# Kernel tuning notes

Hardware: AMD Instinct MI355X
Metric: run time of the kernel (lower is better)

The kernel has to match this reference:

```python
import jax, jax.numpy as jnp
import numpy as np

D_OUT = 512          # full_tensor_dims[0]
VIEW_DIMS = (512, 512, 512)
RANK = 32
BATCH = 4096


def _xavier(key, shape):
    # xavier-style init: scale by sqrt(2 / (fan_in + fan_out)) over first/last dims
    fan_in, fan_out = shape[0] * shape[1], shape[2]
    scale = jnp.sqrt(2.0 / (fan_in + fan_out)).astype(jnp.float32)
    return jax.random.normal(key, shape, dtype=jnp.float32) * scale


def setup_inputs() -> dict:
    key = jax.random.key(0)
    ks = jax.random.split(key, 8)
    X0 = jax.random.normal(ks[0], (VIEW_DIMS[0], BATCH), dtype=jnp.float32)
    X1 = jax.random.normal(ks[1], (VIEW_DIMS[1], BATCH), dtype=jnp.float32)
    X2 = jax.random.normal(ks[2], (VIEW_DIMS[2], BATCH), dtype=jnp.float32)
    # TT cores: rank chain [1, 32, 32, 32, 1]
    core0 = _xavier(ks[3], (1, D_OUT, RANK))            # [1, d_out, r1]
    core1 = _xavier(ks[4], (RANK, VIEW_DIMS[0], RANK))  # [r1, d1, r2]
    core2 = _xavier(ks[5], (RANK, VIEW_DIMS[1], RANK))  # [r2, d2, r3]
    core3 = _xavier(ks[6], (RANK, VIEW_DIMS[2], 1))     # [r3, d3, 1]
    return {"X0": X0, "X1": X1, "X2": X2,
            "core0": core0, "core1": core1, "core2": core2, "core3": core3}


def reference(X0, X1, X2, core0, core1, core2, core3):
    # Batched equivalent of the per-sample Python loop in TensorTrain.forward.
    # For each view j: M_j[n] = mode_dot(core_{j+1}^T_{0,2,1}, X_j[:, n], mode=2)
    #   == einsum('adb,dn->nab'), shape [B, r_{j+1}, r_{j+2}]
    Xs = (X0, X1, X2)
    chain_cores = (core1, core2, core3)
    Ms = [jnp.einsum('adb,dn->nab', c, x) for c, x in zip(chain_cores, Xs)]
    # Chain of per-sample matmuls: z = M_0 @ M_1 @ M_2 -> [B, r1, 1]
    acc = Ms[0]
    for M in Ms[1:]:
        acc = jnp.einsum('nab,nbc->nac', acc, M)
    # Z[:, n] = mode_dot(core0, z[:, 0], mode=2)[0, :]
    Z = jnp.einsum('oda,na->dn', core0, acc[:, :, 0])  # [d_out, B]
    return Z


if __name__ == '__main__':
    out = reference(**setup_inputs())
    print(out.shape)
```

## Files before the change

### kernel.cpp

```cpp
#include <hip/hip_runtime.h>

#define D 512
#define B 4096
#define R 32
#define AB 1024

typedef unsigned short ushort_t;
typedef __attribute__((ext_vector_type(8))) short bf16x8;
typedef __attribute__((ext_vector_type(4))) float f32x4;

__device__ __forceinline__ ushort_t f2bf(float f) {
  uint32_t u = __builtin_bit_cast(uint32_t, f);
  u = (u + 0x7FFFu + ((u >> 16) & 1u)) >> 16;
  return (ushort_t)u;
}
__device__ __forceinline__ float bf2f(ushort_t h) {
  uint32_t u = ((uint32_t)h) << 16;
  return __builtin_bit_cast(float, u);
}
__device__ __forceinline__ void gload_lds16(const void* g, void* lds) {
  __builtin_amdgcn_global_load_lds(
      (const __attribute__((address_space(1))) unsigned int*)g,
      (__attribute__((address_space(3))) unsigned int*)lds, 16, 0, 0);
}

__global__ __launch_bounds__(256) void prep(
    const float* __restrict__ X0, const float* __restrict__ X1,
    const float* __restrict__ X2, const float* __restrict__ c1,
    const float* __restrict__ c2, const float* __restrict__ c3,
    ushort_t* __restrict__ Xt, ushort_t* __restrict__ Apack,
    ushort_t* __restrict__ Apack3)
{
  __shared__ __align__(16) char smem[33280];
  const int bid = blockIdx.x, tid = threadIdx.x;

  if (bid < 1536) {
    float (*T)[65] = (float(*)[65])smem;
    const int v = bid / 512, tile = bid % 512;
    const float* __restrict__ X = (v == 0) ? X0 : ((v == 1) ? X1 : X2);
    ushort_t* __restrict__ O = Xt + (size_t)v * B * D;
    const int n0 = (tile & 63) * 64, d0 = (tile >> 6) * 64;
#pragma unroll
    for (int i = 0; i < 16; ++i) {
      int e = i * 256 + tid;
      T[e >> 6][e & 63] = X[(size_t)(d0 + (e >> 6)) * B + n0 + (e & 63)];
    }
    __syncthreads();
#pragma unroll
    for (int i = 0; i < 2; ++i) {
      int ch = i * 256 + tid;
      int nr = ch >> 3, dc = (ch & 7) * 8;
      ushort_t w[8];
#pragma unroll
      for (int q = 0; q < 8; ++q) w[q] = f2bf(T[dc + q][nr]);
      *(bf16x8*)&O[(size_t)(n0 + nr) * D + d0 + dc] = *(bf16x8*)w;
    }
  } else if (bid < 1600) {
    ushort_t (*T)[D + 8] = (ushort_t(*)[D + 8])smem;
    const int ja = bid - 1536, j = ja >> 5, a = ja & 31;
    const float* __restrict__ c = j ? c2 : c1;
#pragma unroll
    for (int i = 0; i < 64; ++i) {
      int e = i * 256 + tid;
      T[e & 31][e >> 5] = f2bf(c[(size_t)a * (D * R) + e]);
    }
    __syncthreads();
#pragma unroll
    for (int i = 0; i < 8; ++i) {
      int ch = i * 256 + tid;
      int b = ch >> 6, off = (ch & 63) * 8;
      ushort_t w[8];
#pragma unroll
      for (int q = 0; q < 8; ++q) w[q] = T[b][off + q];
      *(bf16x8*)&Apack[((size_t)j * AB + a * 32 + b) * D + off] = *(bf16x8*)w;
    }
  } else {
    const int r0 = (bid - 1600) * 16;
#pragma unroll
    for (int i = 0; i < 4; ++i) {
      int ch = i * 256 + tid;
      int rr = r0 + (ch >> 6), off = (ch & 63) * 8;
      ushort_t w[8];
      if (rr < R) {
#pragma unroll
        for (int q = 0; q < 8; ++q) w[q] = f2bf(c3[(size_t)rr * D + off + q]);
      } else {
#pragma unroll
        for (int q = 0; q < 8; ++q) w[q] = 0;
      }
      *(bf16x8*)&Apack3[(size_t)rr * D + off] = *(bf16x8*)w;
    }
  }
}

__global__ __launch_bounds__(256) void gemm_mfma(
    const ushort_t* __restrict__ Apack, const ushort_t* __restrict__ Apack3,
    const ushort_t* __restrict__ Xt, ushort_t* __restrict__ Mt,
    ushort_t* __restrict__ Mt2)
{
  __shared__ __align__(16) ushort_t smem[17408];
  ushort_t* As0 = smem;
  ushort_t* As1 = smem + 4096;
  ushort_t* Bs0 = smem + 8192;
  ushort_t* Bs1 = smem + 12288;

  const int bid = blockIdx.x;
  int j, rb, nb, ldc;
  const ushort_t *Ag, *Bg;
  ushort_t* C;
  if (bid < 512) {
    j = bid >> 8; int w = bid & 255; rb = w >> 5; nb = w & 31;
    Ag = Xt + (size_t)j * B * D;
    Bg = Apack + (size_t)j * AB * D;
    C  = Mt + (size_t)j * B * AB;  ldc = AB;
  } else {
    j = 2; rb = 0; nb = bid - 512;
    Ag = Xt + (size_t)2 * B * D;
    Bg = Apack3;
    C  = Mt2;  ldc = 128;
  }

  const int tid = threadIdx.x;
  const int lane = tid & 63, wid = tid >> 6;
  const int wr = wid >> 1, wc = wid & 1;
  const int nBase = nb * 128;
  const int rBase = rb * 128;

  const int t0 = wid * 128 + lane, t1 = t0 + 64;
  const int r0 = t0 >> 2, u0 = (t0 & 3) ^ (r0 & 3);
  const int r1 = t1 >> 2, u1 = (t1 & 3) ^ (r1 & 3);
  const ushort_t* gA0 = Ag + (size_t)(nBase + r0) * D + u0 * 8;
  const ushort_t* gA1 = Ag + (size_t)(nBase + r1) * D + u1 * 8;
  const ushort_t* gB0 = Bg + (size_t)(rBase + r0) * D + u0 * 8;
  const ushort_t* gB1 = Bg + (size_t)(rBase + r1) * D + u1 * 8;
  const int lq0 = wid * 1024, lq1 = wid * 1024 + 512;

  int aoff[4], boff[4];
#pragma unroll
  for (int m = 0; m < 4; ++m) {
    int row = wr * 64 + m * 16 + (lane & 15);
    aoff[m] = row * 32 + (((lane >> 4) ^ (row & 3)) * 8);
  }
#pragma unroll
  for (int n = 0; n < 4; ++n) {
    int col = wc * 64 + n * 16 + (lane & 15);
    boff[n] = col * 32 + (((lane >> 4) ^ (col & 3)) * 8);
  }

  f32x4 acc[4][4] = {};

  auto stage = [&](ushort_t* Asb, ushort_t* Bsb, int k0) {
    gload_lds16(gA0 + k0, Asb + lq0);
    gload_lds16(gA1 + k0, Asb + lq1);
    gload_lds16(gB0 + k0, Bsb + lq0);
    gload_lds16(gB1 + k0, Bsb + lq1);
  };
  auto compute = [&](const ushort_t* Asb, const ushort_t* Bsb) {
    bf16x8 a[4], b[4];
#pragma unroll
    for (int m = 0; m < 4; ++m) a[m] = *(const bf16x8*)&Asb[aoff[m]];
#pragma unroll
    for (int n = 0; n < 4; ++n) b[n] = *(const bf16x8*)&Bsb[boff[n]];
#pragma unroll
    for (int m = 0; m < 4; ++m)
#pragma unroll
      for (int n = 0; n < 4; ++n)
        acc[m][n] = __builtin_amdgcn_mfma_f32_16x16x32_bf16(a[m], b[n], acc[m][n], 0, 0, 0);
  };

  stage(As0, Bs0, 0);
  __syncthreads();
#pragma unroll 1
  for (int kp = 0; kp < 8; ++kp) {
    stage(As1, Bs1, kp * 64 + 32);
    compute(As0, Bs0);
    __syncthreads();
    if (kp < 7) stage(As0, Bs0, kp * 64 + 64);
    compute(As1, Bs1);
    __syncthreads();
  }

#define TLD 136
  ushort_t* T = smem;
  const int qn = (lane >> 4) << 2;
#pragma unroll
  for (int m = 0; m < 4; ++m)
#pragma unroll
    for (int nn = 0; nn < 4; ++nn) {
      int nl = wr * 64 + m * 16 + qn;
      int rl = wc * 64 + nn * 16 + (lane & 15);
#pragma unroll
      for (int r = 0; r < 4; ++r)
        T[(nl + r) * TLD + rl] = f2bf(acc[m][nn][r]);
    }
  __syncthreads();
#pragma unroll
  for (int i = 0; i < 8; ++i) {
    int nl = i * 16 + (tid >> 4);
    int rl = (tid & 15) * 8;
    bf16x8 v = *(const bf16x8*)&T[nl * TLD + rl];
    *(bf16x8*)&C[(size_t)(nBase + nl) * ldc + rBase + rl] = v;
  }
}

__global__ __launch_bounds__(256) void chain_kernel(
    const ushort_t* __restrict__ Mt, const ushort_t* __restrict__ Mt2,
    float* __restrict__ zt)
{
  __shared__ float ts[4][R];
  const int tid = threadIdx.x;
  const int lane = tid & 63, w = tid >> 6;
  const int h = lane & 1, g = lane >> 1;
  const ushort_t* __restrict__ Mt0 = Mt;
  const ushort_t* __restrict__ Mt1 = Mt + (size_t)B * AB;
  const int nb = blockIdx.x * 8 + w * 2;

#pragma unroll
  for (int s = 0; s < 2; ++s) {
    const int n = nb + s;
    const size_t rowbase = (size_t)n * AB + lane * 16;

    bf16x8 m2a = *(const bf16x8*)&Mt2[(size_t)n * 128 + h * 16];
    bf16x8 m2b = *(const bf16x8*)&Mt2[(size_t)n * 128 + h * 16 + 8];

    bf16x8 m1a = *(const bf16x8*)&Mt1[rowbase];
    bf16x8 m1b = *(const bf16x8*)&Mt1[rowbase + 8];
    bf16x8 m0a = *(const bf16x8*)&Mt0[rowbase];
    bf16x8 m0b = *(const bf16x8*)&Mt0[rowbase + 8];

    float pt = 0.f;
#pragma unroll
    for (int k = 0; k < 8; ++k) pt += bf2f((ushort_t)m1a[k]) * bf2f((ushort_t)m2a[k]);
#pragma unroll
    for (int k = 0; k < 8; ++k) pt += bf2f((ushort_t)m1b[k]) * bf2f((ushort_t)m2b[k]);
    pt += __shfl_xor(pt, 1, 64);
    if (h == 0) ts[w][g] = pt;

    float pz = 0.f;
#pragma unroll
    for (int k = 0; k < 8; ++k) pz += bf2f((ushort_t)m0a[k]) * ts[w][h * 16 + k];
#pragma unroll
    for (int k = 0; k < 8; ++k) pz += bf2f((ushort_t)m0b[k]) * ts[w][h * 16 + 8 + k];
    pz += __shfl_xor(pz, 1, 64);
    if (h == 0) zt[(size_t)n * R + g] = pz;
  }
}

__global__ __launch_bounds__(256) void zgemm(
    const float* __restrict__ zt, const float* __restrict__ core0,
    float* __restrict__ out)
{
  __shared__ float c0s[64][R];
  __shared__ float zs[R][132];
  const int n0 = blockIdx.x * 128, d0 = blockIdx.y * 64;
  const int tid = threadIdx.x;
#pragma unroll
  for (int i = 0; i < 4; ++i) {
    int ch = i * 256 + tid;
    int nr = ch >> 3, a4 = (ch & 7) * 4;
    float4 v = *(const float4*)&zt[(size_t)(n0 + nr) * R + a4];
    zs[a4 + 0][nr] = v.x; zs[a4 + 1][nr] = v.y;
    zs[a4 + 2][nr] = v.z; zs[a4 + 3][nr] = v.w;
  }
#pragma unroll
  for (int i = 0; i < 2; ++i) {
    int ch = i * 256 + tid;
    int rr = ch >> 3, off = (ch & 7) * 4;
    *(float4*)&c0s[rr][off] = *(const float4*)&core0[(size_t)(d0 + rr) * R + off];
  }
  __syncthreads();
  const int tx = tid & 31, ty = tid >> 5;
  float acc[8][4] = {};
  for (int k = 0; k < R; ++k) {
    float4 z4 = *(const float4*)&zs[k][tx * 4];
    float zz[4] = {z4.x, z4.y, z4.z, z4.w};
#pragma unroll
    for (int i = 0; i < 8; ++i) {
      float cv = c0s[ty * 8 + i][k];
#pragma unroll
      for (int jj = 0; jj < 4; ++jj) acc[i][jj] += cv * zz[jj];
    }
  }
#pragma unroll
  for (int i = 0; i < 8; ++i) {
    float4 o = {acc[i][0], acc[i][1], acc[i][2], acc[i][3]};
    *(float4*)&out[(size_t)(d0 + ty * 8 + i) * B + n0 + tx * 4] = o;
  }
}

extern "C" void kernel_launch(void* const* d_in, const int* in_sizes, int n_in,
                              void* d_out, int out_size, void* d_ws, size_t ws_size,
                              hipStream_t stream)
{
  const float* X0    = (const float*)d_in[0];
  const float* X1    = (const float*)d_in[1];
  const float* X2    = (const float*)d_in[2];
  const float* core0 = (const float*)d_in[3];
  const float* core1 = (const float*)d_in[4];
  const float* core2 = (const float*)d_in[5];
  const float* core3 = (const float*)d_in[6];
  float* out = (float*)d_out;

  char* ws = (char*)d_ws;
  ushort_t* Apack  = (ushort_t*)(ws);
  ushort_t* Apack3 = (ushort_t*)(ws + (2u  << 20));
  ushort_t* Xt     = (ushort_t*)(ws + (4u  << 20));
  ushort_t* Mt     = (ushort_t*)(ws + (16u << 20));
  ushort_t* Mt2    = (ushort_t*)(ws + (32u << 20));
  float*    zt     = (float*)   (ws + (33u << 20));

  hipLaunchKernelGGL(prep, dim3(1608), dim3(256), 0, stream,
                     X0, X1, X2, core1, core2, core3, Xt, Apack, Apack3);
  hipLaunchKernelGGL(gemm_mfma, dim3(544), dim3(256), 0, stream,
                     Apack, Apack3, Xt, Mt, Mt2);
  hipLaunchKernelGGL(chain_kernel, dim3(512), dim3(256), 0, stream, Mt, Mt2, zt);
  hipLaunchKernelGGL(zgemm, dim3(32, 8), dim3(256), 0, stream, zt, core0, out);
}
```

Baseline: 112.3 us.

## Fuse M1·M2 contraction into GEMM epilogue and compute M2 directly in prep

The M2 vector (core3 contracted with X2) is now computed in fp32 inside the prep kernel instead of transposing X2 to bf16 and running extra MFMA blocks. The GEMM for view 1 no longer writes its 8 MB bf16 M1 tensor. Its epilogue contracts each tile with M2 and writes only a small fp32 t vector, which the chain kernel then consumes. This cuts global memory traffic and GEMM blocks. The cost is a scalar fp32 GEMV in prep and extra epilogue work in the GEMM.

```diff
diff --git a/kernel.cpp b/kernel.cpp
--- a/kernel.cpp
+++ b/kernel.cpp
@@ -29,15 +29,15 @@
     const float* __restrict__ X2, const float* __restrict__ c1,
     const float* __restrict__ c2, const float* __restrict__ c3,
     ushort_t* __restrict__ Xt, ushort_t* __restrict__ Apack,
-    ushort_t* __restrict__ Apack3)
+    float* __restrict__ m2buf)
 {
   __shared__ __align__(16) char smem[33280];
   const int bid = blockIdx.x, tid = threadIdx.x;
 
-  if (bid < 1536) {
+  if (bid < 1024) {
     float (*T)[65] = (float(*)[65])smem;
-    const int v = bid / 512, tile = bid % 512;
-    const float* __restrict__ X = (v == 0) ? X0 : ((v == 1) ? X1 : X2);
+    const int v = bid >> 9, tile = bid & 511;
+    const float* __restrict__ X = v ? X1 : X0;
     ushort_t* __restrict__ O = Xt + (size_t)v * B * D;
     const int n0 = (tile & 63) * 64, d0 = (tile >> 6) * 64;
 #pragma unroll
@@ -55,9 +55,9 @@
       for (int q = 0; q < 8; ++q) w[q] = f2bf(T[dc + q][nr]);
       *(bf16x8*)&O[(size_t)(n0 + nr) * D + d0 + dc] = *(bf16x8*)w;
     }
-  } else if (bid < 1600) {
+  } else if (bid < 1088) {
     ushort_t (*T)[D + 8] = (ushort_t(*)[D + 8])smem;
-    const int ja = bid - 1536, j = ja >> 5, a = ja & 31;
+    const int ja = bid - 1024, j = ja >> 5, a = ja & 31;
     const float* __restrict__ c = j ? c2 : c1;
 #pragma unroll
     for (int i = 0; i < 64; ++i) {
@@ -75,28 +75,47 @@
       *(bf16x8*)&Apack[((size_t)j * AB + a * 32 + b) * D + off] = *(bf16x8*)w;
     }
   } else {
-    const int r0 = (bid - 1600) * 16;
-#pragma unroll
-    for (int i = 0; i < 4; ++i) {
-      int ch = i * 256 + tid;
-      int rr = r0 + (ch >> 6), off = (ch & 63) * 8;
-      ushort_t w[8];
-      if (rr < R) {
-#pragma unroll
-        for (int q = 0; q < 8; ++q) w[q] = f2bf(c3[(size_t)rr * D + off + q]);
-      } else {
-#pragma unroll
-        for (int q = 0; q < 8; ++q) w[q] = 0;
+    float (*Xs)[32] = (float(*)[32])smem;
+    float (*mst)[36] = (float(*)[36])(smem + 64 * 32 * 4);
+    const int n0 = (bid - 1088) * 32;
+    const int cc = tid >> 3, nq = tid & 7;
+    float acc[4] = {};
+    for (int d0 = 0; d0 < D; d0 += 64) {
+      __syncthreads();
+#pragma unroll
+      for (int i = 0; i < 8; ++i) {
+        int e = i * 256 + tid;
+        Xs[e >> 5][e & 31] = X2[(size_t)(d0 + (e >> 5)) * B + n0 + (e & 31)];
       }
-      *(bf16x8*)&Apack3[(size_t)rr * D + off] = *(bf16x8*)w;
+      __syncthreads();
+#pragma unroll 4
+      for (int d4 = 0; d4 < 64; d4 += 4) {
+        float4 w4 = *(const float4*)&c3[(size_t)cc * D + d0 + d4];
+        float ww[4] = {w4.x, w4.y, w4.z, w4.w};
+#pragma unroll
+        for (int dd = 0; dd < 4; ++dd) {
+          float4 x = *(const float4*)&Xs[d4 + dd][nq * 4];
+          acc[0] += ww[dd] * x.x; acc[1] += ww[dd] * x.y;
+          acc[2] += ww[dd] * x.z; acc[3] += ww[dd] * x.w;
+        }
+      }
+    }
+    __syncthreads();
+#pragma unroll
+    for (int i = 0; i < 4; ++i) mst[nq * 4 + i][cc] = acc[i];
+    __syncthreads();
+    {
+      int nl = tid >> 3, c4 = (tid & 7) * 4;
+      float4 v = {mst[nl][c4], mst[nl][c4 + 1], mst[nl][c4 + 2], mst[nl][c4 + 3]};
+      *(float4*)&m2buf[(size_t)(n0 + nl) * R + c4] = v;
     }
   }
 }
 
 __global__ __launch_bounds__(256) void gemm_mfma(
-    const ushort_t* __restrict__ Apack, const ushort_t* __restrict__ Apack3,
-    const ushort_t* __restrict__ Xt, ushort_t* __restrict__ Mt,
-    ushort_t* __restrict__ Mt2)
+    const ushort_t* __restrict__ Apack, const ushort_t* __restrict__ Xt,
+    const float* __restrict__ m2buf, ushort_t* __restrict__ Mt0,
+    float* __restrict__ tbuf)
 {
   __shared__ __align__(16) ushort_t smem[17408];
   ushort_t* As0 = smem;
@@ -105,20 +124,10 @@
   ushort_t* Bs1 = smem + 12288;
 
   const int bid = blockIdx.x;
-  int j, rb, nb, ldc;
-  const ushort_t *Ag, *Bg;
-  ushort_t* C;
-  if (bid < 512) {
-    j = bid >> 8; int w = bid & 255; rb = w >> 5; nb = w & 31;
-    Ag = Xt + (size_t)j * B * D;
-    Bg = Apack + (size_t)j * AB * D;
-    C  = Mt + (size_t)j * B * AB;  ldc = AB;
-  } else {
-    j = 2; rb = 0; nb = bid - 512;
-    Ag = Xt + (size_t)2 * B * D;
-    Bg = Apack3;
-    C  = Mt2;  ldc = 128;
-  }
+  const int j = (bid >= 256);
+  const int w = bid & 255, rb = w >> 5, nb = w & 31;
+  const ushort_t* __restrict__ Ag = Xt + (size_t)j * B * D;
+  const ushort_t* __restrict__ Bg = Apack + (size_t)j * AB * D;
 
   const int tid = threadIdx.x;
   const int lane = tid & 63, wid = tid >> 6;
@@ -194,25 +203,47 @@
         T[(nl + r) * TLD + rl] = f2bf(acc[m][nn][r]);
     }
   __syncthreads();
-#pragma unroll
-  for (int i = 0; i < 8; ++i) {
-    int nl = i * 16 + (tid >> 4);
-    int rl = (tid & 15) * 8;
-    bf16x8 v = *(const bf16x8*)&T[nl * TLD + rl];
-    *(bf16x8*)&C[(size_t)(nBase + nl) * ldc + rBase + rl] = v;
-  }
-}
-
-__global__ __launch_bounds__(256) void chain_kernel(
-    const ushort_t* __restrict__ Mt, const ushort_t* __restrict__ Mt2,
+
+  if (j == 0) {
+#pragma unroll
+    for (int i = 0; i < 8; ++i) {
+      int nl = i * 16 + (tid >> 4);
+      int rl = (tid & 15) * 8;
+      bf16x8 v = *(const bf16x8*)&T[nl * TLD + rl];
+      *(bf16x8*)&Mt0[(size_t)(nBase + nl) * AB + rBase + rl] = v;
+    }
+  } else {
+    const int nloc = tid & 127, bh = tid >> 7;
+    const int ng = nBase + nloc;
+    float m2f[32];
+#pragma unroll
+    for (int q = 0; q < 8; ++q) {
+      float4 v = *(const float4*)&m2buf[(size_t)ng * R + q * 4];
+      m2f[q * 4 + 0] = v.x; m2f[q * 4 + 1] = v.y;
+      m2f[q * 4 + 2] = v.z; m2f[q * 4 + 3] = v.w;
+    }
+#pragma unroll
+    for (int bb = 0; bb < 2; ++bb) {
+      int bl = bh * 2 + bb;
+      float t = 0.f;
+#pragma unroll
+      for (int q = 0; q < 4; ++q) {
+        bf16x8 mv = *(const bf16x8*)&T[nloc * TLD + bl * 32 + q * 8];
+#pragma unroll
+        for (int k = 0; k < 8; ++k) t += bf2f((ushort_t)mv[k]) * m2f[q * 8 + k];
+      }
+      tbuf[(size_t)ng * R + (rBase >> 5) + bl] = t;
+    }
+  }
+}
+
+__global__ __launch_bounds__(256) void chainz(
+    const ushort_t* __restrict__ Mt0, const float* __restrict__ tbuf,
     float* __restrict__ zt)
 {
-  __shared__ float ts[4][R];
   const int tid = threadIdx.x;
   const int lane = tid & 63, w = tid >> 6;
   const int h = lane & 1, g = lane >> 1;
-  const ushort_t* __restrict__ Mt0 = Mt;
-  const ushort_t* __restrict__ Mt1 = Mt + (size_t)B * AB;
   const int nb = blockIdx.x * 8 + w * 2;
 
 #pragma unroll
@@ -220,27 +251,21 @@
     const int n = nb + s;
     const size_t rowbase = (size_t)n * AB + lane * 16;
 
-    bf16x8 m2a = *(const bf16x8*)&Mt2[(size_t)n * 128 + h * 16];
-    bf16x8 m2b = *(const bf16x8*)&Mt2[(size_t)n * 128 + h * 16 + 8];
-
-    bf16x8 m1a = *(const bf16x8*)&Mt1[rowbase];
-    bf16x8 m1b = *(const bf16x8*)&Mt1[rowbase + 8];
+    float tf[16];
+#pragma unroll
+    for (int q = 0; q < 4; ++q) {
+      float4 v = *(const float4*)&tbuf[(size_t)n * R + h * 16 + q * 4];
+      tf[q * 4 + 0] = v.x; tf[q * 4 + 1] = v.y;
+      tf[q * 4 + 2] = v.z; tf[q * 4 + 3] = v.w;
+    }
     bf16x8 m0a = *(const bf16x8*)&Mt0[rowbase];
     bf16x8 m0b = *(const bf16x8*)&Mt0[rowbase + 8];
 
-    float pt = 0.f;
-#pragma unroll
-    for (int k = 0; k < 8; ++k) pt += bf2f((ushort_t)m1a[k]) * bf2f((ushort_t)m2a[k]);
-#pragma unroll
-    for (int k = 0; k < 8; ++k) pt += bf2f((ushort_t)m1b[k]) * bf2f((ushort_t)m2b[k]);
-    pt += __shfl_xor(pt, 1, 64);
-    if (h == 0) ts[w][g] = pt;
-
     float pz = 0.f;
 #pragma unroll
-    for (int k = 0; k < 8; ++k) pz += bf2f((ushort_t)m0a[k]) * ts[w][h * 16 + k];
-#pragma unroll
-    for (int k = 0; k < 8; ++k) pz += bf2f((ushort_t)m0b[k]) * ts[w][h * 16 + 8 + k];
+    for (int k = 0; k < 8; ++k) pz += bf2f((ushort_t)m0a[k]) * tf[k];
+#pragma unroll
+    for (int k = 0; k < 8; ++k) pz += bf2f((ushort_t)m0b[k]) * tf[8 + k];
     pz += __shfl_xor(pz, 1, 64);
     if (h == 0) zt[(size_t)n * R + g] = pz;
   }
@@ -302,17 +327,17 @@
   float* out = (float*)d_out;
 
   char* ws = (char*)d_ws;
-  ushort_t* Apack  = (ushort_t*)(ws);
-  ushort_t* Apack3 = (ushort_t*)(ws + (2u  << 20));
-  ushort_t* Xt     = (ushort_t*)(ws + (4u  << 20));
-  ushort_t* Mt     = (ushort_t*)(ws + (16u << 20));
-  ushort_t* Mt2    = (ushort_t*)(ws + (32u << 20));
-  float*    zt     = (float*)   (ws + (33u << 20));
-
-  hipLaunchKernelGGL(prep, dim3(1608), dim3(256), 0, stream,
-                     X0, X1, X2, core1, core2, core3, Xt, Apack, Apack3);
-  hipLaunchKernelGGL(gemm_mfma, dim3(544), dim3(256), 0, stream,
-                     Apack, Apack3, Xt, Mt, Mt2);
-  hipLaunchKernelGGL(chain_kernel, dim3(512), dim3(256), 0, stream, Mt, Mt2, zt);
+  ushort_t* Apack = (ushort_t*)(ws);
+  ushort_t* Xt    = (ushort_t*)(ws + (2u  << 20));
+  ushort_t* Mt0   = (ushort_t*)(ws + (10u << 20));
+  float*    m2buf = (float*)   (ws + (18u << 20));
+  float*    tbuf  = (float*)   (ws + (19u << 20));
+  float*    zt    = (float*)   (ws + (20u << 20));
+
+  hipLaunchKernelGGL(prep, dim3(1216), dim3(256), 0, stream,
+                     X0, X1, X2, core1, core2, core3, Xt, Apack, m2buf);
+  hipLaunchKernelGGL(gemm_mfma, dim3(512), dim3(256), 0, stream,
+                     Apack, Xt, m2buf, Mt0, tbuf);
+  hipLaunchKernelGGL(chainz, dim3(512), dim3(256), 0, stream, Mt0, tbuf, zt);
   hipLaunchKernelGGL(zgemm, dim3(32, 8), dim3(256), 0, stream, zt, core0, out);
 }
```

New measurement: 123.1 us. 9.7% more time.
